# Performance work log

Hardware: AMD Instinct MI355X
Metric: run time of the kernel (lower is better)

## Reference

```python
import jax, jax.numpy as jnp
import numpy as np

C, E, K, O, R, B = 16, 65536, 5, 64, 98, 256  # channels, events/ch, kernel_size, out_ch, ref_size, batch


def setup_inputs() -> dict:
    key = jax.random.key(0)
    ks = jax.random.split(key, 5)
    pseudo = jax.random.uniform(ks[0], (C, E, 1), dtype=jnp.float32)          # normalized times in [0,1)
    y = jax.random.normal(ks[1], (C, E, 1), dtype=jnp.float32)                # observed values
    ref_idx = jax.random.randint(ks[2], (C, E), 0, R * B, dtype=jnp.int32)    # target row per event
    ref_deg = jnp.ones((C, R * B, 1), dtype=jnp.float32)                      # unused (norm=False)
    weight = jax.random.normal(ks[3], (K, C, O), dtype=jnp.float32) * 0.1     # spline kernel weights
    bias = jax.random.normal(ks[4], (O,), dtype=jnp.float32) * 0.1
    return {"pseudo": pseudo, "y": y, "weight": weight, "bias": bias,
            "ref_idx": ref_idx, "ref_deg": ref_deg, "batch_size": B}


def reference(pseudo, y, weight, bias, ref_idx, ref_deg, batch_size):
    # --- SplineBasis: open linear (degree-1) B-spline over 1-D pseudo in [0,1] ---
    v = pseudo[..., 0] * (K - 1)                 # [C,E], scaled coordinate
    bot = jnp.floor(v)
    frac = v - bot                                # fractional position within knot interval
    i0 = bot.astype(jnp.int32)
    i1 = (i0 + 1) % K                             # wrap only possible when frac == 0 (zero basis weight)
    # --- SplineWeighting: per-channel weight gather (weight[:, c] has in_channels=1) ---
    wC = jnp.transpose(weight, (1, 0, 2))         # [C,K,O]
    cidx = jnp.arange(C)[:, None]                 # [C,1]
    w0 = wC[cidx, i0]                             # [C,E,O]
    w1 = wC[cidx, i1]                             # [C,E,O]
    out = y * ((1.0 - frac)[..., None] * w0 + frac[..., None] * w1)  # [C,E,O]
    # --- scatter_add into [ref_size*batch, O]; norm=False so the per-channel
    # scatter followed by sum over channels fuses into a single scatter-add ---
    conv = jnp.zeros((R * batch_size, O), dtype=out.dtype)
    conv = conv.at[ref_idx.reshape(-1)].add(out.reshape(-1, O))
    conv = conv.reshape(batch_size, R, O).transpose(0, 2, 1)  # [B,O,R]
    return conv + bias[:, None]
```

## Files before the change

### kernel.cpp

```cpp
#include <hip/hip_runtime.h>

constexpr int C = 16;
constexpr int E = 65536;
constexpr int K = 5;
constexpr int O = 64;
constexpr int R = 98;
constexpr int B = 256;
constexpr int RB = R * B;
constexpr int NEV = C * E;
constexpr int KC = K * C;

constexpr int SPAD = 84;
constexpr int WPAD = 84;
constexpr int NBIN = 256;

constexpr int NBLKA = 256;
constexpr int TPBA  = 1024;
constexpr int CAP   = 48;
constexpr int NRJ7  = 7;

__device__ __forceinline__ unsigned bf16rne(float f) {
    unsigned u = __float_as_uint(f);
    return (u + 0x7fffu + ((u >> 16) & 1u)) >> 16;
}

__global__ void __launch_bounds__(1024)
bin_events_kernel(const float4* __restrict__ pseudo4,
                  const float4* __restrict__ y4,
                  const int4*   __restrict__ ref4,
                  unsigned*     __restrict__ count,
                  uint2*        __restrict__ rec)
{
    __shared__ unsigned cnt[NBIN];

    const int t = threadIdx.x;
    if (t < NBIN) cnt[t] = 0;
    __syncthreads();

    const int blk = blockIdx.x;
    const int q0  = blk * TPBA + t;
    const float4 p4 = pseudo4[q0];
    const float4 w4 = y4[q0];
    const int4   r4 = ref4[q0];
    const int c = (q0 * 4) >> 16;

    const float* pp = (const float*)&p4;
    const float* yy = (const float*)&w4;
    const int*   rr = (const int*)&r4;

#pragma unroll
    for (int j = 0; j < 4; ++j) {
        const float p    = pp[j];
        const float yv   = yy[j];
        const int   ridx = rr[j];

        const unsigned b = (unsigned)ridx / (unsigned)R;
        const int r      = ridx - (int)b * R;

        const float v    = p * (float)(K - 1);
        const float bot  = floorf(v);
        const float frac = v - bot;
        const int   i0   = (int)bot;

        const unsigned meta = (unsigned)(r * SPAD + i0 * C + c);
        const unsigned lo   = bf16rne(yv * (1.0f - frac)) | (bf16rne(yv * frac) << 16);

        const unsigned s = atomicAdd(&cnt[b], 1u);
        if (s < (unsigned)CAP)
            rec[((size_t)(blk * NBIN) + b) * CAP + s] = make_uint2(lo, meta);
    }
    __syncthreads();

    if (t < NBIN) count[blk * NBIN + t] = cnt[t];
}

__global__ void __launch_bounds__(1024)
fused_gemm_kernel(const unsigned* __restrict__ count,
                  const uint2*    __restrict__ rec,
                  const float*    __restrict__ weight,
                  const float*    __restrict__ bias,
                  float*          __restrict__ out)
{
    __shared__ __align__(16) float s_S[R * SPAD];
    __shared__ __align__(16) float s_w[O * WPAD];
    __shared__ unsigned s_cnt[NBLKA];

    const int b = blockIdx.x;
    const int t = threadIdx.x;

    for (int i = t; i < (R * SPAD) / 4 + 1; i += 1024) {
        const int i4 = i * 4;
        if (i4 < R * SPAD)
            *(float4*)&s_S[i4] = make_float4(0.f, 0.f, 0.f, 0.f);
    }
    for (int idx = t; idx < KC * O; idx += 1024) {
        const int kc = idx >> 6;
        const int o  = idx & 63;
        s_w[o * WPAD + kc] = weight[idx];
    }
    if (t < NBLKA) s_cnt[t] = count[t * NBIN + b];
    __syncthreads();

    {
        const int cell = t & 255;
        const int q    = t >> 8;
        const unsigned n = min(s_cnt[cell], (unsigned)CAP);
        const uint2* rb = rec + ((size_t)(cell * NBIN) + b) * CAP;
        for (unsigned s = q; s < n; s += 4) {
            const uint2 e = rb[s];
            const float v0 = __uint_as_float(e.x << 16);
            const float v1 = __uint_as_float(e.x & 0xffff0000u);
            const unsigned off = e.y;
            atomicAdd(&s_S[off], v0);
            atomicAdd(&s_S[off + C], v1);
        }
    }
    __syncthreads();

    const int oo = t >> 4;
    const int rg = t & 15;

    float acc[NRJ7];
#pragma unroll
    for (int j = 0; j < NRJ7; ++j) acc[j] = 0.0f;

    for (int k4 = 0; k4 < KC / 4; ++k4) {
        const float4 w = *(const float4*)&s_w[oo * WPAD + 4 * k4];
#pragma unroll
        for (int j = 0; j < NRJ7; ++j) {
            const int r = rg + 16 * j;
            if (r < R) {
                const float4 sv = *(const float4*)&s_S[r * SPAD + 4 * k4];
                acc[j] += w.x * sv.x + w.y * sv.y + w.z * sv.z + w.w * sv.w;
            }
        }
    }

    const float bs = bias[oo];
    float* orow = out + ((size_t)b * O + oo) * R;
#pragma unroll
    for (int j = 0; j < NRJ7; ++j) {
        const int r = rg + 16 * j;
        if (r < R) orow[r] = acc[j] + bs;
    }
}

constexpr int NRJ = 13;

__global__ void accum_S8_kernel(const float* __restrict__ pseudo,
                                const float* __restrict__ y,
                                const int*   __restrict__ ref_idx,
                                float*       __restrict__ S8)
{
    const int tid  = blockIdx.x * blockDim.x + threadIdx.x;
    const int l    = tid & 1;
    const int grp  = tid >> 1;
    const int ngrp = (gridDim.x * blockDim.x) >> 1;

    for (int ev = grp; ev < NEV; ev += ngrp) {
        const int   c    = ev >> 16;
        const float p    = pseudo[ev];
        const float yy   = y[ev];
        const int   ridx = ref_idx[ev];

        const float v    = p * (float)(K - 1);
        const float bot  = floorf(v);
        const float frac = v - bot;
        const int   i0   = (int)bot;

        const float val = l ? yy * frac : yy * (1.0f - frac);
        atomicAdd(&S8[(((size_t)ridx * C) + c) * 8 + i0 + l], val);
    }
}

__global__ void __launch_bounds__(256)
gemm_out_kernel(const float* __restrict__ S8,
                const float* __restrict__ weight,
                const float* __restrict__ bias,
                float*       __restrict__ out)
{
    __shared__ __align__(16) float s_S[R * SPAD];
    __shared__ __align__(16) float s_w[O * WPAD];

    const int b = blockIdx.x;
    const float* S8b = S8 + (size_t)b * R * C * 8;

    for (int idx = threadIdx.x; idx < R * C * 8; idx += 256) {
        const int r   = idx >> 7;
        const int rem = idx & 127;
        const int c   = rem >> 3;
        const int i   = rem & 7;
        if (i < K) s_S[r * SPAD + i * C + c] = S8b[idx];
    }
    for (int idx = threadIdx.x; idx < KC * O; idx += 256) {
        const int kc = idx >> 6;
        const int o  = idx & 63;
        s_w[o * WPAD + kc] = weight[idx];
    }
    __syncthreads();

    const int oo = threadIdx.x >> 3;
    const int rg = threadIdx.x & 7;

    float accL[NRJ], accH[NRJ];
#pragma unroll
    for (int j = 0; j < NRJ; ++j) { accL[j] = 0.0f; accH[j] = 0.0f; }

    for (int k4 = 0; k4 < KC / 4; ++k4) {
        const float4 wl = *(const float4*)&s_w[oo * WPAD + 4 * k4];
        const float4 wh = *(const float4*)&s_w[(oo + 32) * WPAD + 4 * k4];
#pragma unroll
        for (int j = 0; j < NRJ; ++j) {
            const int r = rg + 8 * j;
            if (r < R) {
                const float4 sv = *(const float4*)&s_S[r * SPAD + 4 * k4];
                accL[j] += wl.x * sv.x + wl.y * sv.y + wl.z * sv.z + wl.w * sv.w;
                accH[j] += wh.x * sv.x + wh.y * sv.y + wh.z * sv.z + wh.w * sv.w;
            }
        }
    }

    const float bL = bias[oo];
    const float bH = bias[oo + 32];
    float* orowL = out + ((size_t)b * O + oo) * R;
    float* orowH = out + ((size_t)b * O + oo + 32) * R;
#pragma unroll
    for (int j = 0; j < NRJ; ++j) {
        const int r = rg + 8 * j;
        if (r < R) {
            orowL[r] = accL[j] + bL;
            orowH[r] = accH[j] + bH;
        }
    }
}

__global__ void init_out_kernel(const float* __restrict__ bias,
                                float*       __restrict__ out)
{
    const int idx = blockIdx.x * blockDim.x + threadIdx.x;
    if (idx >= B * O * R) return;
    const int o = (idx / R) % O;
    out[idx] = bias[o];
}

__global__ void scatter_direct_kernel(const float* __restrict__ pseudo,
                                      const float* __restrict__ y,
                                      const float* __restrict__ weight,
                                      const int*   __restrict__ ref_idx,
                                      float*       __restrict__ out)
{
    __shared__ float sw[KC * O];
    for (int i = threadIdx.x; i < KC * O; i += blockDim.x)
        sw[i] = weight[i];
    __syncthreads();

    const int lane   = threadIdx.x & 63;
    const int wave   = (blockIdx.x * blockDim.x + threadIdx.x) >> 6;
    const int nwaves = (gridDim.x * blockDim.x) >> 6;

    for (int ev = wave; ev < NEV; ev += nwaves) {
        const int   c    = ev >> 16;
        const float p    = pseudo[ev];
        const float yy   = y[ev];
        const int   ridx = ref_idx[ev];
        const int   b    = ridx / R;
        const int   r    = ridx - b * R;

        const float v    = p * (float)(K - 1);
        const float bot  = floorf(v);
        const float frac = v - bot;
        int i0 = (int)bot;
        int i1 = i0 + 1;
        if (i1 == K) i1 = 0;

        const float w0 = sw[(i0 * C + c) * O + lane];
        const float w1 = sw[(i1 * C + c) * O + lane];
        atomicAdd(&out[((size_t)b * O + lane) * R + r],
                  yy * ((1.0f - frac) * w0 + frac * w1));
    }
}

extern "C" void kernel_launch(void* const* d_in, const int* in_sizes, int n_in,
                              void* d_out, int out_size, void* d_ws, size_t ws_size,
                              hipStream_t stream)
{
    const float* pseudo  = (const float*)d_in[0];
    const float* y       = (const float*)d_in[1];
    const float* weight  = (const float*)d_in[2];
    const float* bias    = (const float*)d_in[3];
    const int*   ref_idx = (const int*)d_in[4];

    float* out = (float*)d_out;

    const size_t cnt_bytes = (size_t)NBLKA * NBIN * sizeof(unsigned);
    const size_t rec_bytes = (size_t)NBLKA * NBIN * CAP * sizeof(uint2);
    const size_t pri_bytes = cnt_bytes + rec_bytes;
    const size_t S8_bytes  = (size_t)RB * C * 8 * sizeof(float);

    if (ws_size >= pri_bytes) {
        unsigned* count = (unsigned*)d_ws;
        uint2*    rec   = (uint2*)((char*)d_ws + cnt_bytes);
        bin_events_kernel<<<NBLKA, TPBA, 0, stream>>>(
            (const float4*)pseudo, (const float4*)y, (const int4*)ref_idx,
            count, rec);
        fused_gemm_kernel<<<NBIN, 1024, 0, stream>>>(
            count, rec, weight, bias, out);
    } else if (ws_size >= S8_bytes) {
        float* S8 = (float*)d_ws;
        hipMemsetAsync(S8, 0, S8_bytes, stream);
        accum_S8_kernel<<<4096, 256, 0, stream>>>(pseudo, y, ref_idx, S8);
        gemm_out_kernel<<<B, 256, 0, stream>>>(S8, weight, bias, out);
    } else {
        const int fin_threads = 256;
        const int fin_blocks = (B * O * R + fin_threads - 1) / fin_threads;
        init_out_kernel<<<fin_blocks, fin_threads, 0, stream>>>(bias, out);
        scatter_direct_kernel<<<4096, 256, 0, stream>>>(
            pseudo, y, weight, ref_idx, out);
    }
}
```

Baseline: 37.80 us.

## Use 512-thread gemm blocks with 4x output register tiling and nontemporal record stores

The binning kernel now packs each record into a single 64-bit word and writes records and counts with nontemporal stores, aiming to reduce cache pollution on write-once data. The fused gemm kernel drops to 512 threads per block. Each thread handles half as many scatter iterations' worth of stride, and only 256 threads run the GEMM with four output channels each, so every shared-memory S load is reused across four weight rows. In exchange, the GEMM phase leaves half the block idle and raises per-thread register pressure.

```diff
diff --git a/kernel.cpp b/kernel.cpp
--- a/kernel.cpp
+++ b/kernel.cpp
@@ -29,7 +29,7 @@
                   const float4* __restrict__ y4,
                   const int4*   __restrict__ ref4,
                   unsigned*     __restrict__ count,
-                  uint2*        __restrict__ rec)
+                  unsigned long long* __restrict__ rec)
 {
     __shared__ unsigned cnt[NBIN];
 
@@ -64,19 +64,23 @@
 
         const unsigned meta = (unsigned)(r * SPAD + i0 * C + c);
         const unsigned lo   = bf16rne(yv * (1.0f - frac)) | (bf16rne(yv * frac) << 16);
+        const unsigned long long r64 =
+            ((unsigned long long)meta << 32) | (unsigned long long)lo;
 
         const unsigned s = atomicAdd(&cnt[b], 1u);
         if (s < (unsigned)CAP)
-            rec[((size_t)(blk * NBIN) + b) * CAP + s] = make_uint2(lo, meta);
-    }
-    __syncthreads();
-
-    if (t < NBIN) count[blk * NBIN + t] = cnt[t];
-}
-
-__global__ void __launch_bounds__(1024)
+            __builtin_nontemporal_store(
+                r64, &rec[((size_t)(blk * NBIN) + b) * CAP + s]);
+    }
+    __syncthreads();
+
+    if (t < NBIN)
+        __builtin_nontemporal_store(cnt[t], &count[blk * NBIN + t]);
+}
+
+__global__ void __launch_bounds__(512)
 fused_gemm_kernel(const unsigned* __restrict__ count,
-                  const uint2*    __restrict__ rec,
+                  const unsigned long long* __restrict__ rec,
                   const float*    __restrict__ weight,
                   const float*    __restrict__ bias,
                   float*          __restrict__ out)
@@ -88,12 +92,12 @@
     const int b = blockIdx.x;
     const int t = threadIdx.x;
 
-    for (int i = t; i < (R * SPAD) / 4 + 1; i += 1024) {
+    for (int i = t; i < (R * SPAD) / 4 + 1; i += 512) {
         const int i4 = i * 4;
         if (i4 < R * SPAD)
             *(float4*)&s_S[i4] = make_float4(0.f, 0.f, 0.f, 0.f);
     }
-    for (int idx = t; idx < KC * O; idx += 1024) {
+    for (int idx = t; idx < KC * O; idx += 512) {
         const int kc = idx >> 6;
         const int o  = idx & 63;
         s_w[o * WPAD + kc] = weight[idx];
@@ -103,45 +107,61 @@
 
     {
         const int cell = t & 255;
-        const int q    = t >> 8;
+        const int half = t >> 8;
         const unsigned n = min(s_cnt[cell], (unsigned)CAP);
-        const uint2* rb = rec + ((size_t)(cell * NBIN) + b) * CAP;
-        for (unsigned s = q; s < n; s += 4) {
-            const uint2 e = rb[s];
-            const float v0 = __uint_as_float(e.x << 16);
-            const float v1 = __uint_as_float(e.x & 0xffff0000u);
-            const unsigned off = e.y;
+        const unsigned long long* rb = rec + ((size_t)(cell * NBIN) + b) * CAP;
+        for (unsigned s = half; s < n; s += 2) {
+            const unsigned long long e = rb[s];
+            const unsigned lo  = (unsigned)e;
+            const unsigned off = (unsigned)(e >> 32);
+            const float v0 = __uint_as_float(lo << 16);
+            const float v1 = __uint_as_float(lo & 0xffff0000u);
             atomicAdd(&s_S[off], v0);
             atomicAdd(&s_S[off + C], v1);
         }
     }
     __syncthreads();
 
-    const int oo = t >> 4;
-    const int rg = t & 15;
-
-    float acc[NRJ7];
-#pragma unroll
-    for (int j = 0; j < NRJ7; ++j) acc[j] = 0.0f;
-
-    for (int k4 = 0; k4 < KC / 4; ++k4) {
-        const float4 w = *(const float4*)&s_w[oo * WPAD + 4 * k4];
-#pragma unroll
-        for (int j = 0; j < NRJ7; ++j) {
-            const int r = rg + 16 * j;
-            if (r < R) {
-                const float4 sv = *(const float4*)&s_S[r * SPAD + 4 * k4];
-                acc[j] += w.x * sv.x + w.y * sv.y + w.z * sv.z + w.w * sv.w;
+    if (t < 256) {
+        const int rg = t & 15;
+        const int og = t >> 4;
+
+        float acc[4][NRJ7];
+#pragma unroll
+        for (int q = 0; q < 4; ++q)
+#pragma unroll
+            for (int j = 0; j < NRJ7; ++j) acc[q][j] = 0.0f;
+
+#pragma unroll 4
+        for (int k4 = 0; k4 < KC / 4; ++k4) {
+            const float4 w0 = *(const float4*)&s_w[(og     ) * WPAD + 4 * k4];
+            const float4 w1 = *(const float4*)&s_w[(og + 16) * WPAD + 4 * k4];
+            const float4 w2 = *(const float4*)&s_w[(og + 32) * WPAD + 4 * k4];
+            const float4 w3 = *(const float4*)&s_w[(og + 48) * WPAD + 4 * k4];
+#pragma unroll
+            for (int j = 0; j < NRJ7; ++j) {
+                const int r = rg + 16 * j;
+                if (r < R) {
+                    const float4 sv = *(const float4*)&s_S[r * SPAD + 4 * k4];
+                    acc[0][j] += w0.x * sv.x + w0.y * sv.y + w0.z * sv.z + w0.w * sv.w;
+                    acc[1][j] += w1.x * sv.x + w1.y * sv.y + w1.z * sv.z + w1.w * sv.w;
+                    acc[2][j] += w2.x * sv.x + w2.y * sv.y + w2.z * sv.z + w2.w * sv.w;
+                    acc[3][j] += w3.x * sv.x + w3.y * sv.y + w3.z * sv.z + w3.w * sv.w;
+                }
             }
         }
-    }
-
-    const float bs = bias[oo];
-    float* orow = out + ((size_t)b * O + oo) * R;
-#pragma unroll
-    for (int j = 0; j < NRJ7; ++j) {
-        const int r = rg + 16 * j;
-        if (r < R) orow[r] = acc[j] + bs;
+
+#pragma unroll
+        for (int q = 0; q < 4; ++q) {
+            const int o = og + 16 * q;
+            const float bs = bias[o];
+            float* orow = out + ((size_t)b * O + o) * R;
+#pragma unroll
+            for (int j = 0; j < NRJ7; ++j) {
+                const int r = rg + 16 * j;
+                if (r < R) orow[r] = acc[q][j] + bs;
+            }
+        }
     }
 }
 
@@ -293,17 +313,17 @@
     float* out = (float*)d_out;
 
     const size_t cnt_bytes = (size_t)NBLKA * NBIN * sizeof(unsigned);
-    const size_t rec_bytes = (size_t)NBLKA * NBIN * CAP * sizeof(uint2);
+    const size_t rec_bytes = (size_t)NBLKA * NBIN * CAP * 8;
     const size_t pri_bytes = cnt_bytes + rec_bytes;
     const size_t S8_bytes  = (size_t)RB * C * 8 * sizeof(float);
 
     if (ws_size >= pri_bytes) {
         unsigned* count = (unsigned*)d_ws;
-        uint2*    rec   = (uint2*)((char*)d_ws + cnt_bytes);
+        unsigned long long* rec = (unsigned long long*)((char*)d_ws + cnt_bytes);
         bin_events_kernel<<<NBLKA, TPBA, 0, stream>>>(
             (const float4*)pseudo, (const float4*)y, (const int4*)ref_idx,
             count, rec);
-        fused_gemm_kernel<<<NBIN, 1024, 0, stream>>>(
+        fused_gemm_kernel<<<NBIN, 512, 0, stream>>>(
             count, rec, weight, bias, out);
     } else if (ws_size >= S8_bytes) {
         float* S8 = (float*)d_ws;
```

Result: slower. 55.36 us (+46.4%).
